# Performance work log

Measured on AMD Instinct MI355X. Metric: run time of the kernel, lower is better.

## Reference

```python
import jax, jax.numpy as jnp
import numpy as np

HEAD_DIM = 128
NUM_HEADS = 16
HIDDEN = 2048
SEQ = 4096
ROPE_THETA = 10000.0
RMS_EPS = 1e-6


def _rms_norm(x, w, eps=RMS_EPS):
    # per-head RMSNorm over last dim (head_dim)
    var = jnp.mean(jnp.square(x), axis=-1, keepdims=True)
    return x * jax.lax.rsqrt(var + eps) * w


def _rope_cos_sin(position_ids, dim=HEAD_DIM, theta=ROPE_THETA):
    freqs = 1.0 / theta ** (jnp.arange(0, dim, 2, dtype=jnp.float32) / dim)  # [dim/2]
    ang = position_ids.astype(jnp.float32)[:, None] * freqs[None, :]  # [S, dim/2]
    return jnp.cos(ang), jnp.sin(ang)


def _apply_rope(x, cos, sin):
    # x: [S, H, D]; pairs (x0, x1) along last dim act as complex numbers
    S, H, D = x.shape
    xr = x.astype(jnp.float32).reshape(S, H, D // 2, 2)
    x0, x1 = xr[..., 0], xr[..., 1]
    c = cos[:, None, :]  # [S, 1, D/2]
    s = sin[:, None, :]
    o0 = x0 * c - x1 * s
    o1 = x0 * s + x1 * c
    out = jnp.stack((o0, o1), axis=-1).reshape(S, H, D)
    return out.astype(x.dtype)


def setup_inputs() -> dict:
    key = jax.random.key(0)
    ks = jax.random.split(key, 8)
    std = 0.02
    return {
        "hidden_states": jax.random.normal(ks[0], (SEQ, HIDDEN), dtype=jnp.float32),
        "position_ids": jnp.arange(SEQ, dtype=jnp.int64 if jax.config.jax_enable_x64 else jnp.int32),
        "wq": jax.random.normal(ks[1], (HIDDEN, HIDDEN), dtype=jnp.float32) * std,
        "wk": jax.random.normal(ks[2], (HIDDEN, HIDDEN), dtype=jnp.float32) * std,
        "wv": jax.random.normal(ks[3], (HIDDEN, HIDDEN), dtype=jnp.float32) * std,
        "wo": jax.random.normal(ks[4], (HIDDEN, HIDDEN), dtype=jnp.float32) * std,
        "q_norm_w": jnp.ones((HEAD_DIM,), dtype=jnp.float32),
        "k_norm_w": jnp.ones((HEAD_DIM,), dtype=jnp.float32),
    }


def reference(hidden_states, position_ids, wq, wk, wv, wo, q_norm_w, k_norm_w):
    S = hidden_states.shape[0]
    # QKV projections (NormalLinear: x @ weight)
    xq = hidden_states @ wq
    xk = hidden_states @ wk
    xv = hidden_states @ wv
    # split heads: [S, H, D]
    xq = xq.reshape(S, NUM_HEADS, HEAD_DIM)
    xk = xk.reshape(S, NUM_HEADS, HEAD_DIM)
    xv = xv.reshape(S, NUM_HEADS, HEAD_DIM)
    # per-head qk RMSNorm
    xq = _rms_norm(xq, q_norm_w)
    xk = _rms_norm(xk, k_norm_w)
    # rotary embedding
    cos, sin = _rope_cos_sin(position_ids)
    xq = _apply_rope(xq, cos, sin)
    xk = _apply_rope(xk, cos, sin)
    # scaled dot-product attention (no mask), TNH layout
    context = jax.nn.dot_product_attention(xq, xk, xv)
    # merge heads and output projection (dropout p=0 -> identity)
    out = context.reshape(S, NUM_HEADS * HEAD_DIM) @ wo
    return out
```

## Files before the change

kernel.cpp:

```cpp
#include <hip/hip_runtime.h>

typedef __bf16 bf16x8 __attribute__((ext_vector_type(8)));
typedef __bf16 bf16x4 __attribute__((ext_vector_type(4)));
typedef float  f32x4  __attribute__((ext_vector_type(4)));
typedef float  f32x16 __attribute__((ext_vector_type(16)));
typedef unsigned u32x4 __attribute__((ext_vector_type(4)));

#define MFMA16(A, B, C) __builtin_amdgcn_mfma_f32_16x16x32_bf16(A, B, C, 0, 0, 0)
#define MFMA32(A, B, C) __builtin_amdgcn_mfma_f32_32x32x16_bf16(A, B, C, 0, 0, 0)
#define AS1 __attribute__((address_space(1)))
#define AS3 __attribute__((address_space(3)))

#if __has_builtin(__builtin_amdgcn_exp2f)
#define EXP2F(x) __builtin_amdgcn_exp2f(x)
#else
#define EXP2F(x) exp2f(x)
#endif

__device__ __forceinline__ unsigned pk_bf16(float lo, float hi) {
    unsigned r;
    asm("v_cvt_pk_bf16_f32 %0, %1, %2" : "=v"(r) : "v"(lo), "v"(hi));
    return r;
}

__global__ __launch_bounds__(256) void prep(const float* __restrict__ hs,
                                            const float* __restrict__ wq,
                                            const float* __restrict__ wk,
                                            const float* __restrict__ wv,
                                            const float* __restrict__ wo,
                                            __bf16* __restrict__ xb,
                                            __bf16* __restrict__ wqkvtb,
                                            __bf16* __restrict__ wotb) {
    __shared__ float tile[32][33];
    const int z = blockIdx.z;
    const int tx = threadIdx.x, ty = threadIdx.y;
    if (z == 4) {
        const int t = ty * 32 + tx;
        size_t bid = (size_t)blockIdx.y * 64 + blockIdx.x;
        size_t base = bid * 2048 + t * 4;
        for (int c = 0; c < 2; ++c) {
            float4 v = *(const float4*)(hs + base + c * 1024);
            bf16x4 o;
            o.x = (__bf16)v.x; o.y = (__bf16)v.y; o.z = (__bf16)v.z; o.w = (__bf16)v.w;
            *(bf16x4*)(xb + base + c * 1024) = o;
        }
        return;
    }
    const float* src = (z == 0) ? wq : (z == 1) ? wk : (z == 2) ? wv : wo;
    __bf16* dst = (z < 3) ? (wqkvtb + (size_t)z * 2048 * 2048) : wotb;
    int x0 = blockIdx.x * 32, y0 = blockIdx.y * 32;
    for (int r = 0; r < 4; ++r)
        tile[ty + 8 * r][tx] = src[(size_t)(y0 + ty + 8 * r) * 2048 + x0 + tx];
    __syncthreads();
    for (int r = 0; r < 4; ++r)
        dst[(size_t)(x0 + ty + 8 * r) * 2048 + y0 + tx] = (__bf16)tile[tx][ty + 8 * r];
}

__global__ __launch_bounds__(256) void rope_vt(const __bf16* __restrict__ qkv,
                                               const float* __restrict__ qw,
                                               const float* __restrict__ kw,
                                               const int* __restrict__ pos_ids,
                                               __bf16* __restrict__ qhb,
                                               __bf16* __restrict__ khb,
                                               __bf16* __restrict__ vtb) {
    __shared__ __bf16 tile[32][33];
    if (blockIdx.y < 32) {
        int u = threadIdx.x >> 6, lane = threadIdx.x & 63;
        int s = blockIdx.x * 4 + u;
        int slot = blockIdx.y;
        bool isQ = slot < 16;
        int h = slot & 15;
        size_t base = (size_t)s * 6144 + (isQ ? 0 : 2048) + h * 128 + lane * 2;
        float x0 = (float)qkv[base], x1 = (float)qkv[base + 1];
        float ss = x0 * x0 + x1 * x1;
        for (int m = 1; m < 64; m <<= 1) ss += __shfl_xor(ss, m);
        float rr = rsqrtf(ss * (1.0f / 128.0f) + 1e-6f);
        const float* wp = isQ ? qw : kw;
        float n0 = x0 * rr * wp[lane * 2], n1 = x1 * rr * wp[lane * 2 + 1];
        float freq = EXP2F(-(float)lane * 0.2076205059004571f);
        float ang = (float)pos_ids[s] * freq;
        float sn, cs;
        sincosf(ang, &sn, &cs);
        float o0 = n0 * cs - n1 * sn;
        float o1 = n0 * sn + n1 * cs;
        if (isQ) { o0 *= 0.12751744416196178f; o1 *= 0.12751744416196178f; }
        __bf16* dst = (isQ ? qhb : khb) + (size_t)h * 4096 * 128 + (size_t)s * 128 + lane * 2;
        dst[0] = (__bf16)o0; dst[1] = (__bf16)o1;
    } else {
        int linear = (blockIdx.y - 32) * 1024 + blockIdx.x;
        int h = linear >> 9, rem = linear & 511;
        int s0 = (rem & 127) * 32, d0 = (rem >> 7) * 32;
        int tx = threadIdx.x & 31, ty = threadIdx.x >> 5;
        for (int r = 0; r < 4; ++r)
            tile[ty + 8 * r][tx] = qkv[(size_t)(s0 + ty + 8 * r) * 6144 + 4096 + h * 128 + d0 + tx];
        __syncthreads();
        for (int r = 0; r < 4; ++r)
            vtb[(size_t)h * 128 * 4096 + (size_t)(d0 + ty + 8 * r) * 4096 + s0 + tx] = tile[tx][ty + 8 * r];
    }
}

template <bool F32OUT>
__global__ __launch_bounds__(256) void gemm_bt(const __bf16* __restrict__ A, int lda,
                                               const __bf16* __restrict__ Bt, int ldb,
                                               void* __restrict__ Cout, int ldc, int K) {
    __shared__ __bf16 as[3][128][32];
    __shared__ __bf16 bs[3][128][32];
    const int m0 = blockIdx.x * 128, n0 = blockIdx.y * 128;
    const int t = threadIdx.x;
    const int lane = t & 63, w = t >> 6;
    const int wm = (w >> 1) * 64, wn = (w & 1) * 64;
    const int ln = lane & 15, quad = lane >> 4;
    auto as3 = (AS3 uint32_t*)&as[0][0][0];
    auto bs3 = (AS3 uint32_t*)&bs[0][0][0];
    f32x4 acc[4][4] = {};

#define G_STAGE(buf, k0)                                                             \
    for (int c = 0; c < 2; ++c) {                                                    \
        int g = c * 256 + t;                                                         \
        int row = g >> 2, kc = g & 3;                                                \
        __builtin_amdgcn_global_load_lds(                                            \
            (const AS1 uint32_t*)&A[(size_t)(m0 + row) * lda + (k0) + kc * 8],       \
            as3 + (buf) * 2048 + c * 1024 + w * 256, 16, 0, 0);                      \
        __builtin_amdgcn_global_load_lds(                                            \
            (const AS1 uint32_t*)&Bt[(size_t)(n0 + row) * ldb + (k0) + kc * 8],      \
            bs3 + (buf) * 2048 + c * 1024 + w * 256, 16, 0, 0);                      \
    }

    const int nk = K >> 5;
    G_STAGE(0, 0)
    G_STAGE(1, 32)
    for (int kt = 0; kt < nk; ++kt) {
        const int nxt = kt + 2;
        if (nxt < nk) {
            G_STAGE(nxt % 3, nxt * 32)
            asm volatile("s_waitcnt vmcnt(8)" ::: "memory");
        } else if (nxt == nk) {
            asm volatile("s_waitcnt vmcnt(4)" ::: "memory");
        } else {
            asm volatile("s_waitcnt vmcnt(0)" ::: "memory");
        }
        __builtin_amdgcn_s_barrier();
        const int b = kt % 3;
        bf16x8 af[4], bfr[4];
        for (int i = 0; i < 4; ++i) af[i] = *(const bf16x8*)&as[b][wm + i * 16 + ln][quad * 8];
        for (int j = 0; j < 4; ++j) bfr[j] = *(const bf16x8*)&bs[b][wn + j * 16 + ln][quad * 8];
        for (int i = 0; i < 4; ++i)
            for (int j = 0; j < 4; ++j)
                acc[i][j] = MFMA16(af[i], bfr[j], acc[i][j]);
        __builtin_amdgcn_s_barrier();
    }
#undef G_STAGE

    for (int i = 0; i < 4; ++i)
        for (int j = 0; j < 4; ++j)
            for (int r = 0; r < 4; ++r) {
                int row = m0 + wm + i * 16 + quad * 4 + r;
                int col = n0 + wn + j * 16 + ln;
                if (F32OUT) ((float*)Cout)[(size_t)row * ldc + col] = acc[i][j][r];
                else        ((__bf16*)Cout)[(size_t)row * ldc + col] = (__bf16)acc[i][j][r];
            }
}

#define SOFTMAX_PV(sac, ktv)                                                        \
    {                                                                               \
        float p[16];                                                                \
        _Pragma("unroll")                                                           \
        for (int r = 0; r < 16; ++r) { p[r] = EXP2F((sac)[r]); rs += p[r]; }        \
        unsigned a00 = pk_bf16(p[0], p[1]),  a01 = pk_bf16(p[2], p[3]);             \
        unsigned b00 = pk_bf16(p[4], p[5]),  b01 = pk_bf16(p[6], p[7]);             \
        unsigned a10 = pk_bf16(p[8], p[9]),  a11 = pk_bf16(p[10], p[11]);           \
        unsigned b10 = pk_bf16(p[12], p[13]), b11 = pk_bf16(p[14], p[15]);          \
        auto s00 = __builtin_amdgcn_permlane32_swap(a00, b00, false, false);        \
        auto s01 = __builtin_amdgcn_permlane32_swap(a01, b01, false, false);        \
        auto s10 = __builtin_amdgcn_permlane32_swap(a10, b10, false, false);        \
        auto s11 = __builtin_amdgcn_permlane32_swap(a11, b11, false, false);        \
        u32x4 w0, w1;                                                               \
        w0[0] = s00[0]; w0[1] = s01[0]; w0[2] = s00[1]; w0[3] = s01[1];             \
        w1[0] = s10[0]; w1[1] = s11[0]; w1[2] = s10[1]; w1[3] = s11[1];             \
        bf16x8 pf0 = __builtin_bit_cast(bf16x8, w0);                                \
        bf16x8 pf1 = __builtin_bit_cast(bf16x8, w1);                                \
        __builtin_amdgcn_s_setprio(1);                                              \
        _Pragma("unroll")                                                           \
        for (int dt = 0; dt < 4; ++dt) {                                            \
            int vrow = dt * 32 + q32;                                               \
            int co0 = (((ktv) * 2 + 0) << 1) | hi;                                  \
            int co1 = (((ktv) * 2 + 1) << 1) | hi;                                  \
            bf16x8 vf0 = *(const bf16x8*)(vsb + vrow * 128 + ((co0 ^ (q32 & 7)) << 4)); \
            bf16x8 vf1 = *(const bf16x8*)(vsb + vrow * 128 + ((co1 ^ (q32 & 7)) << 4)); \
            oacc[dt] = MFMA32(pf0, vf0, oacc[dt]);                                  \
            oacc[dt] = MFMA32(pf1, vf1, oacc[dt]);                                  \
        }                                                                           \
        __builtin_amdgcn_s_setprio(0);                                              \
    }

__global__ __launch_bounds__(256) void flash_attn(const __bf16* __restrict__ Q,
                                                  const __bf16* __restrict__ Kb,
                                                  const __bf16* __restrict__ Vt,
                                                  __bf16* __restrict__ ctx) {
    __shared__ __bf16 kbuf[2][64][128];
    __shared__ __bf16 vbuf[2][128][64];
    __shared__ float lred[4][32];

    int bid = blockIdx.x + (int)gridDim.x * blockIdx.y;
    int swz = (bid & 7) * 64 + (bid >> 3);
    const int h  = swz >> 5;
    const int m0 = (swz & 31) * 128;

    const int t = threadIdx.x;
    const int lane = t & 63, w = t >> 6;
    const int q32 = lane & 31, hi = lane >> 5;
    const __bf16* Qh = Q + (size_t)h * 4096 * 128;
    const __bf16* Kh = Kb + (size_t)h * 4096 * 128;
    const __bf16* Vh = Vt + (size_t)h * 128 * 4096;

    const int kcc = (t & 15) ^ ((t >> 4) & 7);
    const int vcc = (t & 7) ^ ((t >> 3) & 7);
    auto kb3 = (AS3 uint32_t*)&kbuf[0][0][0];
    auto vb3 = (AS3 uint32_t*)&vbuf[0][0][0];
    const char* kbase = (const char*)&kbuf[0][0][0];
    const char* vbase = (const char*)&vbuf[0][0][0];

    bf16x8 qf[8];
    for (int half = 0; half < 2; ++half) {
        for (int i = 0; i < 4; ++i) {
            int row = (t >> 4) + i * 16;
            *(uint4*)&kbuf[0][row][(t & 15) * 8] =
                *(const uint4*)&Qh[(size_t)(m0 + half * 64 + row) * 128 + kcc * 8];
        }
        __syncthreads();
        if ((w >> 1) == half) {
            int r = (w & 1) * 32 + q32;
            #pragma unroll
            for (int dc = 0; dc < 8; ++dc)
                qf[dc] = *(const bf16x8*)(kbase + r * 256 + ((((dc << 1) | hi) ^ (r & 7)) << 4));
        }
        __syncthreads();
    }

#define STAGE_KV(buf, tile)                                                          \
    for (int i = 0; i < 4; ++i) {                                                    \
        int krow = (t >> 4) + i * 16;                                                \
        __builtin_amdgcn_global_load_lds(                                            \
            (const AS1 uint32_t*)&Kh[(size_t)((tile) * 64 + krow) * 128 + kcc * 8],  \
            kb3 + (buf) * 4096 + (w * 64 + i * 256) * 4, 16, 0, 0);                  \
        int vrow = (t >> 3) + i * 32;                                                \
        __builtin_amdgcn_global_load_lds(                                            \
            (const AS1 uint32_t*)&Vh[(size_t)vrow * 4096 + (tile) * 64 + vcc * 8],   \
            vb3 + (buf) * 4096 + (w * 64 + i * 256) * 4, 16, 0, 0);                  \
    }

    STAGE_KV(0, 0)
    __syncthreads();

    f32x16 oacc[4] = {};
    float rs = 0.0f;
    int cur = 0;

    f32x16 mC16;
    #pragma unroll
    for (int e = 0; e < 16; ++e) mC16[e] = -16.5f;

    for (int kb = 0; kb < 64; ++kb) {
        if (kb + 1 < 64) { STAGE_KV(cur ^ 1, kb + 1) }

        const char* ksb = kbase + cur * 16384;
        const char* vsb = vbase + cur * 16384;

        f32x16 sacc0, sacc1;
        __builtin_amdgcn_s_setprio(1);
        {
            int co = hi;
            bf16x8 kf0 = *(const bf16x8*)(ksb + q32 * 256        + ((co ^ (q32 & 7)) << 4));
            bf16x8 kf1 = *(const bf16x8*)(ksb + (32 + q32) * 256 + ((co ^ (q32 & 7)) << 4));
            sacc0 = MFMA32(kf0, qf[0], mC16);
            sacc1 = MFMA32(kf1, qf[0], mC16);
        }
        #pragma unroll
        for (int dc = 1; dc < 8; ++dc) {
            int co = (dc << 1) | hi;
            bf16x8 kf0 = *(const bf16x8*)(ksb + q32 * 256        + ((co ^ (q32 & 7)) << 4));
            bf16x8 kf1 = *(const bf16x8*)(ksb + (32 + q32) * 256 + ((co ^ (q32 & 7)) << 4));
            sacc0 = MFMA32(kf0, qf[dc], sacc0);
            sacc1 = MFMA32(kf1, qf[dc], sacc1);
        }
        __builtin_amdgcn_s_setprio(0);

        SOFTMAX_PV(sacc0, 0)
        SOFTMAX_PV(sacc1, 1)

        __syncthreads();
        cur ^= 1;
    }
#undef STAGE_KV

    float rt = rs + __shfl_xor(rs, 32);
    if (hi == 0) lred[w][q32] = rt;
    __syncthreads();
    float inv[16];
    #pragma unroll
    for (int r = 0; r < 16; ++r)
        inv[r] = 1.0f / lred[w][(r & 3) + 8 * (r >> 2) + 4 * hi];
    #pragma unroll
    for (int dt = 0; dt < 4; ++dt)
        #pragma unroll
        for (int r = 0; r < 16; ++r) {
            int row = m0 + w * 32 + (r & 3) + 8 * (r >> 2) + 4 * hi;
            int col = h * 128 + dt * 32 + q32;
            ctx[(size_t)row * 2048 + col] = (__bf16)(oacc[dt][r] * inv[r]);
        }
}

extern "C" void kernel_launch(void* const* d_in, const int* in_sizes, int n_in,
                              void* d_out, int out_size, void* d_ws, size_t ws_size,
                              hipStream_t stream) {
    const float* hs  = (const float*)d_in[0];
    const int*   pos = (const int*)d_in[1];
    const float* wq  = (const float*)d_in[2];
    const float* wk  = (const float*)d_in[3];
    const float* wv  = (const float*)d_in[4];
    const float* wo  = (const float*)d_in[5];
    const float* qw  = (const float*)d_in[6];
    const float* kw  = (const float*)d_in[7];

    char* ws = (char*)d_ws;
    const size_t MB = 1024 * 1024;
    __bf16* xb     = (__bf16*)(ws + 0);
    __bf16* wqkvtb = (__bf16*)(ws + 16 * MB);
    __bf16* qhb    = (__bf16*)(ws + 0);
    __bf16* khb    = (__bf16*)(ws + 16 * MB);
    __bf16* vtb    = (__bf16*)(ws + 32 * MB);
    __bf16* qkvb   = (__bf16*)(ws + 48 * MB);
    __bf16* ctxb   = (__bf16*)(ws + 48 * MB);
    __bf16* wotb   = (__bf16*)(ws + 96 * MB);

    prep<<<dim3(64, 64, 5), dim3(32, 8), 0, stream>>>(hs, wq, wk, wv, wo, xb, wqkvtb, wotb);

    gemm_bt<false><<<dim3(32, 48), 256, 0, stream>>>(xb, 2048, wqkvtb, 2048, qkvb, 6144, 2048);

    rope_vt<<<dim3(1024, 40), 256, 0, stream>>>(qkvb, qw, kw, pos, qhb, khb, vtb);

    flash_attn<<<dim3(32, 16), 256, 0, stream>>>(qhb, khb, vtb, ctxb);

    gemm_bt<true><<<dim3(32, 16), 256, 0, stream>>>(ctxb, 2048, wotb, 2048, d_out, 2048, 2048);
}
```

Measured before the change: 472.5 us.

## Use BK=64 double-buffered GEMM tiles with XOR-swizzled LDS layout

The GEMM k-tile grows from 32 to 64 and the three-stage buffer becomes a two-stage double buffer. Global-to-LDS loads now place 16-byte chunks using an XOR swizzle of column chunk against row, and the fragment reads apply the matching swizzle to avoid LDS bank conflicts on the wider rows. The aim is to halve the barrier and loop overhead per unit of K and to remove bank conflicts. In exchange, prefetch depth drops from two tiles ahead to one.

```diff
diff --git a/kernel.cpp b/kernel.cpp
--- a/kernel.cpp
+++ b/kernel.cpp
@@ -103,8 +103,8 @@
 __global__ __launch_bounds__(256) void gemm_bt(const __bf16* __restrict__ A, int lda,
                                                const __bf16* __restrict__ Bt, int ldb,
                                                void* __restrict__ Cout, int ldc, int K) {
-    __shared__ __bf16 as[3][128][32];
-    __shared__ __bf16 bs[3][128][32];
+    __shared__ __bf16 as[2][128][64];
+    __shared__ __bf16 bs[2][128][64];
     const int m0 = blockIdx.x * 128, n0 = blockIdx.y * 128;
     const int t = threadIdx.x;
     const int lane = t & 63, w = t >> 6;
@@ -112,41 +112,54 @@
     const int ln = lane & 15, quad = lane >> 4;
     auto as3 = (AS3 uint32_t*)&as[0][0][0];
     auto bs3 = (AS3 uint32_t*)&bs[0][0][0];
+    const char* abase = (const char*)&as[0][0][0];
+    const char* bbase = (const char*)&bs[0][0][0];
+    const int scc = (t & 7) ^ ((t >> 3) & 7);
     f32x4 acc[4][4] = {};
 
 #define G_STAGE(buf, k0)                                                             \
-    for (int c = 0; c < 2; ++c) {                                                    \
+    for (int c = 0; c < 4; ++c) {                                                    \
         int g = c * 256 + t;                                                         \
-        int row = g >> 2, kc = g & 3;                                                \
+        int row = g >> 3;                                                            \
         __builtin_amdgcn_global_load_lds(                                            \
-            (const AS1 uint32_t*)&A[(size_t)(m0 + row) * lda + (k0) + kc * 8],       \
-            as3 + (buf) * 2048 + c * 1024 + w * 256, 16, 0, 0);                      \
+            (const AS1 uint32_t*)&A[(size_t)(m0 + row) * lda + (k0) + scc * 8],      \
+            as3 + (buf) * 4096 + g * 4, 16, 0, 0);                                   \
         __builtin_amdgcn_global_load_lds(                                            \
-            (const AS1 uint32_t*)&Bt[(size_t)(n0 + row) * ldb + (k0) + kc * 8],      \
-            bs3 + (buf) * 2048 + c * 1024 + w * 256, 16, 0, 0);                      \
-    }
-
-    const int nk = K >> 5;
+            (const AS1 uint32_t*)&Bt[(size_t)(n0 + row) * ldb + (k0) + scc * 8],     \
+            bs3 + (buf) * 4096 + g * 4, 16, 0, 0);                                   \
+    }
+
+    const int nt = K >> 6;
     G_STAGE(0, 0)
-    G_STAGE(1, 32)
-    for (int kt = 0; kt < nk; ++kt) {
-        const int nxt = kt + 2;
-        if (nxt < nk) {
-            G_STAGE(nxt % 3, nxt * 32)
+    for (int kt = 0; kt < nt; ++kt) {
+        if (kt + 1 < nt) {
+            G_STAGE((kt + 1) & 1, (kt + 1) * 64)
             asm volatile("s_waitcnt vmcnt(8)" ::: "memory");
-        } else if (nxt == nk) {
-            asm volatile("s_waitcnt vmcnt(4)" ::: "memory");
         } else {
             asm volatile("s_waitcnt vmcnt(0)" ::: "memory");
         }
         __builtin_amdgcn_s_barrier();
-        const int b = kt % 3;
-        bf16x8 af[4], bfr[4];
-        for (int i = 0; i < 4; ++i) af[i] = *(const bf16x8*)&as[b][wm + i * 16 + ln][quad * 8];
-        for (int j = 0; j < 4; ++j) bfr[j] = *(const bf16x8*)&bs[b][wn + j * 16 + ln][quad * 8];
-        for (int i = 0; i < 4; ++i)
-            for (int j = 0; j < 4; ++j)
-                acc[i][j] = MFMA16(af[i], bfr[j], acc[i][j]);
+        const char* ab = abase + (kt & 1) * 16384;
+        const char* bb = bbase + (kt & 1) * 16384;
+        #pragma unroll
+        for (int ks = 0; ks < 2; ++ks) {
+            bf16x8 af[4], bfr[4];
+            #pragma unroll
+            for (int i = 0; i < 4; ++i) {
+                int rr = wm + i * 16 + ln;
+                af[i] = *(const bf16x8*)(ab + rr * 128 + (((ks * 4 + quad) ^ (ln & 7)) << 4));
+            }
+            #pragma unroll
+            for (int j = 0; j < 4; ++j) {
+                int rr = wn + j * 16 + ln;
+                bfr[j] = *(const bf16x8*)(bb + rr * 128 + (((ks * 4 + quad) ^ (ln & 7)) << 4));
+            }
+            #pragma unroll
+            for (int i = 0; i < 4; ++i)
+                #pragma unroll
+                for (int j = 0; j < 4; ++j)
+                    acc[i][j] = MFMA16(af[i], bfr[j], acc[i][j]);
+        }
         __builtin_amdgcn_s_barrier();
     }
 #undef G_STAGE
```

Result: faster. 457.1 us (median of 3 runs) (-3.3%).
